# Kernel tuning notes

Measured on AMD Instinct MI355X. Metric: run time of the kernel, lower is better.

Reference implementation:

```python
import jax, jax.numpy as jnp
import numpy as np

# Dimensions (see shape_source): batch, tokens, input dim, attention feature dim, output dim
B, T, D_IN, D_ATTN, D_OUT = 8, 2048, 512, 8, 512
# Weight scale keeps Q,K entries ~N(0, 0.5^2) so scores**power stays finite in fp32
W_SCALE = 0.5 / np.sqrt(D_IN)


def setup_inputs() -> dict:
    key = jax.random.key(0)
    k1, k2, k3, k4 = jax.random.split(key, 4)
    Input = jax.random.normal(k1, (B, T, D_IN), dtype=jnp.float32)
    W_q = jax.random.normal(k2, (D_IN, D_ATTN), dtype=jnp.float32) * W_SCALE
    W_k = jax.random.normal(k3, (D_IN, D_ATTN), dtype=jnp.float32) * W_SCALE
    W_v = jax.random.normal(k4, (D_IN, D_OUT), dtype=jnp.float32) * W_SCALE
    return {"Input": Input, "W_q": W_q, "W_k": W_k, "W_v": W_v, "power": D_ATTN}


def reference(Input, W_q, W_k, W_v, power):
    # QKV projections (torch.mm applied per token)
    Q = jnp.einsum('btd,df->btf', Input, W_q)   # [B,T,D_ATTN]
    K = jnp.einsum('btd,df->btf', Input, W_k)   # [B,T,D_ATTN]
    V = jnp.einsum('btd,do->bto', Input, W_v)   # [B,T,D_OUT]
    # Non-standard score transform: elementwise power by Attention.Feature.Num
    scores = jnp.einsum('btf,bsf->bts', Q, K) ** power  # [B,T,T]
    A = jax.nn.softmax(scores, axis=2)
    # Weighted sum of values
    return jnp.einsum('bts,bso->bto', A, V)  # [B,T,D_OUT]
```

## Files before the change

### kernel.cpp

```cpp
#include <hip/hip_runtime.h>
#include <hip/hip_bf16.h>
#include <stdint.h>


typedef float f32x4_t __attribute__((ext_vector_type(4)));
typedef short s16x8_t __attribute__((ext_vector_type(8)));
typedef unsigned int u32;

static __device__ __forceinline__ unsigned short f2bf(float x){
  union { float f; u32 u; } v; v.f = x;
  return (unsigned short)((v.u + 0x7FFFu + ((v.u >> 16) & 1u)) >> 16);
}

static __device__ __forceinline__ u32 pk2bf(float a, float b){
  __hip_bfloat162 h = __float22bfloat162_rn(float2{a, b});
  union { __hip_bfloat162 h2; u32 u; } c; c.h2 = h;
  return c.u;
}

static __device__ __forceinline__ void gload16(const void* g, void* l){
  __builtin_amdgcn_global_load_lds((const __attribute__((address_space(1))) u32*)g,
                                   (__attribute__((address_space(3))) u32*)l, 16, 0, 0);
}

static __device__ __forceinline__ float rfl(float x){
  return __uint_as_float(__builtin_amdgcn_readfirstlane(__float_as_uint(x)));
}

static __device__ __forceinline__ float dot8(const float* q, const float4& a, const float4& b){
  float s = q[0] * a.x;
  s = fmaf(q[1], a.y, s); s = fmaf(q[2], a.z, s); s = fmaf(q[3], a.w, s);
  s = fmaf(q[4], b.x, s); s = fmaf(q[5], b.y, s); s = fmaf(q[6], b.z, s);
  s = fmaf(q[7], b.w, s);
  return s;
}

__global__ __launch_bounds__(256) void k_wvT(const float* __restrict__ Wv,
                                             unsigned short* __restrict__ WvT){
  __shared__ __align__(16) float tile[64][68];
  const int t = threadIdx.x;
  const int dbase = (blockIdx.x >> 3) * 64;
  const int cbase = (blockIdx.x & 7) * 64;
  {
    const int dl = t >> 2, cq = (t & 3) * 16;
    const float* src = Wv + (size_t)(dbase + dl) * 512 + cbase + cq;
#pragma unroll
    for (int i = 0; i < 16; i += 4){
      float4 v = *(const float4*)(src + i);
      tile[dl][cq + i + 0] = v.x; tile[dl][cq + i + 1] = v.y;
      tile[dl][cq + i + 2] = v.z; tile[dl][cq + i + 3] = v.w;
    }
  }
  __syncthreads();
  const int cl = t >> 2, dq = (t & 3) * 16;
  __align__(16) unsigned short o[16];
#pragma unroll
  for (int i = 0; i < 16; ++i) o[i] = f2bf(tile[dq + i][cl]);
  unsigned short* dst = WvT + (size_t)(cbase + cl) * 512 + dbase + dq;
  *(uint4*)dst = *(const uint4*)o;
  *(uint4*)(dst + 8) = *(const uint4*)(o + 8);
}

__global__ __launch_bounds__(256) void k_fused(const float* __restrict__ In,
                                               const float* __restrict__ Wq,
                                               const float* __restrict__ Wk,
                                               const unsigned short* __restrict__ WvT,
                                               float* __restrict__ Qo,
                                               float* __restrict__ Kt,
                                               unsigned short* __restrict__ Vg){
  __shared__ __align__(16) char smem[65536];
  const int t = threadIdx.x;
  if (blockIdx.x < 1024){
    float* wt = (float*)smem;
    float* inT = (float*)(smem + 32768);
    const float* Inb = In + (size_t)blockIdx.x * 16 * 512;
#pragma unroll
    for (int i = 0; i < 8; ++i)
      gload16(Inb + (i * 256 + t) * 4, (char*)inT + (i * 256 + t) * 16);
#pragma unroll
    for (int i = 0; i < 16; i += 4){
      float4 vq = *(const float4*)(Wq + t * 16 + i);
      float4 vk = *(const float4*)(Wk + t * 16 + i);
      const float* pq = &vq.x;
      const float* pk = &vk.x;
#pragma unroll
      for (int j = 0; j < 4; ++j){
        int flat = t * 16 + i + j;
        int d = flat >> 3, f = flat & 7;
        wt[f * 512 + ((((d >> 2) ^ f) << 2) | (d & 3))] = pq[j];
        int fk = f + 8;
        wt[fk * 512 + ((((d >> 2) ^ (fk & 7)) << 2) | (d & 3))] = pk[j];
      }
    }
    __syncthreads();
    const int tokl = t >> 4;
    const int f = t & 15;
    const float* inrow = inT + tokl * 512;
    const float* wrow = &wt[f * 512];
    const int swz = f & 7;
    double acc = 0.0;
    for (int cb = 0; cb < 128; cb += 8){
      float part = 0.f;
#pragma unroll
      for (int c = cb; c < cb + 8; ++c){
        float4 x = *(const float4*)(inrow + c * 4);
        float4 ww = *(const float4*)(wrow + ((c ^ swz) << 2));
        part = fmaf(x.x, ww.x, part); part = fmaf(x.y, ww.y, part);
        part = fmaf(x.z, ww.z, part); part = fmaf(x.w, ww.w, part);
      }
      acc += (double)part;
    }
    float r = (float)acc;
    const int tok = (int)blockIdx.x * 16 + tokl;
    if (f < 8) Qo[(size_t)tok * 8 + f] = r;
    else {
      const int bq = tok >> 11, kk = tok & 2047;
      const int key = kk & 127, d = f - 8;
      Kt[(size_t)bq * 16384 + (size_t)(kk >> 7) * 1024
         + ((key & 1) * 2 + (d >> 2)) * 256 + (key >> 1) * 4 + (d & 3)] = r;
    }
    return;
  }
  char* Ab = smem;
  char* Bb = smem + 16384;
  char* Img = smem + 32768;
  const int vb = (int)blockIdx.x - 1024;
  const int w = t >> 6, lane = t & 63;
  const int mt = vb >> 2, nt = vb & 3;
  const int wm = w >> 1, wn = w & 1;
  const int asub = lane & 3;
  int arow[2], acr[2];
#pragma unroll
  for (int i = 0; i < 2; ++i){
    arow[i] = (w * 2 + i) * 16 + (lane >> 2);
    acr[i]  = asub ^ ((arow[i] >> 1) & 3);
  }
  f32x4_t acc[4][4];
#pragma unroll
  for (int m = 0; m < 4; ++m)
#pragma unroll
    for (int n = 0; n < 4; ++n)
      acc[m][n] = (f32x4_t){0.f, 0.f, 0.f, 0.f};

  auto stageB = [&](int kk, int sel){
#pragma unroll
    for (int i = 0; i < 2; ++i){
      int id = w * 2 + i;
      const unsigned short* gb = WvT + (size_t)(nt * 128 + arow[i]) * 512 + kk * 32 + acr[i] * 8;
      gload16(gb, Bb + sel * 8192 + id * 1024);
    }
  };
  auto loadA = [&](int kk, float4* x, float4* y){
#pragma unroll
    for (int i = 0; i < 2; ++i){
      const float* ga = In + (size_t)(mt * 128 + arow[i]) * 512 + kk * 32 + acr[i] * 8;
      x[i] = *(const float4*)ga;
      y[i] = *(const float4*)(ga + 4);
    }
  };
  auto writeA = [&](const float4* x, const float4* y, int sel){
#pragma unroll
    for (int i = 0; i < 2; ++i){
      __align__(16) unsigned short pk[8] = {
        f2bf(x[i].x), f2bf(x[i].y), f2bf(x[i].z), f2bf(x[i].w),
        f2bf(y[i].x), f2bf(y[i].y), f2bf(y[i].z), f2bf(y[i].w)};
      *(uint4*)(Ab + sel * 8192 + arow[i] * 64 + asub * 16) = *(const uint4*)pk;
    }
  };
  {
    float4 x[2], y[2];
    loadA(0, x, y);
    stageB(0, 0);
    writeA(x, y, 0);
    __syncthreads();
  }
  for (int kk = 0; kk < 16; ++kk){
    const int cur = kk & 1;
    float4 x[2], y[2];
    if (kk < 15){
      loadA(kk + 1, x, y);
      stageB(kk + 1, cur ^ 1);
    }
    s16x8_t a[4], bf[4];
#pragma unroll
    for (int m = 0; m < 4; ++m){
      int row = wm * 64 + m * 16 + (lane & 15);
      int chn = (lane >> 4) ^ ((row >> 1) & 3);
      a[m] = *(const s16x8_t*)(Ab + cur * 8192 + row * 64 + chn * 16);
    }
#pragma unroll
    for (int n = 0; n < 4; ++n){
      int col = wn * 64 + n * 16 + (lane & 15);
      int chn = (lane >> 4) ^ ((col >> 1) & 3);
      bf[n] = *(const s16x8_t*)(Bb + cur * 8192 + col * 64 + chn * 16);
    }
#pragma unroll
    for (int m = 0; m < 4; ++m)
#pragma unroll
      for (int n = 0; n < 4; ++n)
        acc[m][n] = __builtin_amdgcn_mfma_f32_16x16x32_bf16(a[m], bf[n], acc[m][n], 0, 0, 0);
    if (kk < 15) writeA(x, y, cur ^ 1);
    __syncthreads();
  }
#pragma unroll
  for (int m = 0; m < 4; ++m){
    const int ks2 = (wm * 2 + (m >> 1)) & 3;
    const int hi  = (m * 2 + ((lane >> 4) >> 1)) & 3;
    const int lo0 = ((lane >> 4) & 1) * 4;
#pragma unroll
    for (int n = 0; n < 4; ++n){
      const int g_loc = wn * 2 + (n >> 1);
      const int n2 = n & 1;
      const int cl = lane & 15;
      __align__(8) unsigned short pk2[4];
#pragma unroll
      for (int j = 0; j < 4; ++j) pk2[j] = f2bf(acc[m][n][j]);
      int boff = g_loc * 8192 + n2 * 4096 + ks2 * 1024 + hi * 256 + cl * 16 + lo0 * 2;
      *(uint2*)(Img + boff) = *(const uint2*)pk2;
    }
  }
  __syncthreads();
  const int bq = mt >> 4;
  const int kt = mt & 15;
#pragma unroll
  for (int i = 0; i < 8; ++i){
    int G = i * 256 + t;
    unsigned short* dst = Vg + (size_t)bq * 1048576 + (size_t)kt * 65536
                        + nt * 16384 + G * 8;
    *(uint4*)dst = *(const uint4*)(Img + G * 16);
  }
}

__global__ __launch_bounds__(1024) void k_attn(const float* __restrict__ Qg,
                                               const float* __restrict__ Kt,
                                               const unsigned short* __restrict__ Vg,
                                               float* __restrict__ Out){
  __shared__ __align__(16) char smem[102656];
  const int t = threadIdx.x;
  const int g = t >> 6, lane = t & 63;
  const int b = blockIdx.x & 7;
  const int qt = blockIdx.x >> 3;
  const int qbase = qt * 64;

  float q4[4][8];
#pragma unroll
  for (int rr = 0; rr < 4; ++rr){
    const float* Qp = Qg + (size_t)(b * 2048 + qbase + g * 4 + rr) * 8;
    float4 a = *(const float4*)Qp;
    float4 c = *(const float4*)(Qp + 4);
    q4[rr][0] = rfl(a.x); q4[rr][1] = rfl(a.y); q4[rr][2] = rfl(a.z); q4[rr][3] = rfl(a.w);
    q4[rr][4] = rfl(c.x); q4[rr][5] = rfl(c.y); q4[rr][6] = rfl(c.z); q4[rr][7] = rfl(c.w);
  }
  const float* Kp = Kt + (size_t)b * 16384;
  const unsigned short* Vb = Vg + (size_t)b * 1048576;
  char* Klds = smem;
  char* Pb = smem + 65536;
  float* fin = (float*)(smem + 102400);

#pragma unroll
  for (int i = 0; i < 4; ++i)
    gload16(Kp + (size_t)(i * 1024 + t) * 4, Klds + (i * 1024 + t) * 16);
  __syncthreads();

  float mx0 = 0.f, mx1 = 0.f, mx2 = 0.f, mx3 = 0.f;
  {
    const float* kbase = (const float*)Klds + lane * 4;
#pragma unroll 2
    for (int tt = 0; tt < 16; ++tt){
      const float* kb = kbase + tt * 1024;
      float4 r0 = *(const float4*)(kb);
      float4 r1 = *(const float4*)(kb + 256);
      float4 r2 = *(const float4*)(kb + 512);
      float4 r3 = *(const float4*)(kb + 768);
      {
        float s0 = dot8(q4[0], r0, r1), s1 = dot8(q4[0], r2, r3);
        mx0 = fmaxf(mx0, fmaxf(s0 * s0, s1 * s1));
      }
      {
        float s0 = dot8(q4[1], r0, r1), s1 = dot8(q4[1], r2, r3);
        mx1 = fmaxf(mx1, fmaxf(s0 * s0, s1 * s1));
      }
      {
        float s0 = dot8(q4[2], r0, r1), s1 = dot8(q4[2], r2, r3);
        mx2 = fmaxf(mx2, fmaxf(s0 * s0, s1 * s1));
      }
      {
        float s0 = dot8(q4[3], r0, r1), s1 = dot8(q4[3], r2, r3);
        mx3 = fmaxf(mx3, fmaxf(s0 * s0, s1 * s1));
      }
    }
  }
#pragma unroll
  for (int sh = 1; sh < 64; sh <<= 1){
    mx0 = fmaxf(mx0, __shfl_xor(mx0, sh));
    mx1 = fmaxf(mx1, __shfl_xor(mx1, sh));
    mx2 = fmaxf(mx2, __shfl_xor(mx2, sh));
    mx3 = fmaxf(mx3, __shfl_xor(mx3, sh));
  }
  const float LOG2E = 1.44269504f;
  float nme2_0, nme2_1, nme2_2, nme2_3;
  { float s4 = mx0 * mx0; nme2_0 = rfl(-(s4 * s4) * LOG2E); }
  { float s4 = mx1 * mx1; nme2_1 = rfl(-(s4 * s4) * LOG2E); }
  { float s4 = mx2 * mx2; nme2_2 = rfl(-(s4 * s4) * LOG2E); }
  { float s4 = mx3 * mx3; nme2_3 = rfl(-(s4 * s4) * LOG2E); }
  float lp0 = 0.f, lp1 = 0.f, lp2 = 0.f, lp3 = 0.f;

  f32x4_t acc[4][2];
#pragma unroll
  for (int mm = 0; mm < 4; ++mm)
#pragma unroll
    for (int n = 0; n < 2; ++n)
      acc[mm][n] = (f32x4_t){0.f, 0.f, 0.f, 0.f};

  auto scoreRow = [&](int rr, float nme2r, float& lpr,
                      const float4& r0, const float4& r1,
                      const float4& r2, const float4& r3, int sel){
    float s0 = dot8(q4[rr], r0, r1), s1 = dot8(q4[rr], r2, r3);
    float p0, p1;
    { float a2 = s0 * s0; float a4 = a2 * a2; p0 = a4 * a4; }
    { float a2 = s1 * s1; float a4 = a2 * a2; p1 = a4 * a4; }
    float e0 = __builtin_amdgcn_exp2f(fmaf(p0, LOG2E, nme2r));
    float e1 = __builtin_amdgcn_exp2f(fmaf(p1, LOG2E, nme2r));
    lpr += e0 + e1;
    const int row = g * 4 + rr;
    *(u32*)(Pb + sel * 16384 + row * 256
            + ((((lane >> 2) ^ (row & 15))) << 4) + (lane & 3) * 4) = pk2bf(e0, e1);
  };

  {
    const float* kb = (const float*)Klds + lane * 4;
    float4 r0 = *(const float4*)(kb);
    float4 r1 = *(const float4*)(kb + 256);
    float4 r2 = *(const float4*)(kb + 512);
    float4 r3 = *(const float4*)(kb + 768);
    scoreRow(0, nme2_0, lp0, r0, r1, r2, r3, 0);
    scoreRow(1, nme2_1, lp1, r0, r1, r2, r3, 0);
    scoreRow(2, nme2_2, lp2, r0, r1, r2, r3, 0);
    scoreRow(3, nme2_3, lp3, r0, r1, r2, r3, 0);
  }
  __syncthreads();

  for (int tt = 0; tt < 16; ++tt){
    const int sel = tt & 1;
    s16x8_t vf[2][4];
    {
      const unsigned short* vb = Vb + (size_t)tt * 65536 + g * 4096 + lane * 8;
#pragma unroll
      for (int n = 0; n < 2; ++n)
#pragma unroll
        for (int ks = 0; ks < 4; ++ks)
          vf[n][ks] = *(const s16x8_t*)(vb + n * 2048 + ks * 512);
    }
    const bool more = (tt + 1 < 16);
    float4 r0, r1, r2, r3;
    if (more){
      const float* kb = (const float*)Klds + ((tt + 1) & 15) * 1024 + lane * 4;
      r0 = *(const float4*)(kb);
      r1 = *(const float4*)(kb + 256);
      r2 = *(const float4*)(kb + 512);
      r3 = *(const float4*)(kb + 768);
    }
#pragma unroll
    for (int ks = 0; ks < 4; ++ks){
      if (more){
        if (ks == 0) scoreRow(0, nme2_0, lp0, r0, r1, r2, r3, sel ^ 1);
        if (ks == 1) scoreRow(1, nme2_1, lp1, r0, r1, r2, r3, sel ^ 1);
        if (ks == 2) scoreRow(2, nme2_2, lp2, r0, r1, r2, r3, sel ^ 1);
        if (ks == 3) scoreRow(3, nme2_3, lp3, r0, r1, r2, r3, sel ^ 1);
      }
      s16x8_t a[4];
#pragma unroll
      for (int mm = 0; mm < 4; ++mm){
        int r = mm * 16 + (lane & 15);
        int slot = (ks * 4 + (lane >> 4)) ^ (r & 15);
        a[mm] = *(const s16x8_t*)(Pb + sel * 16384 + r * 256 + (slot << 4));
      }
      __builtin_amdgcn_s_setprio(1);
#pragma unroll
      for (int mm = 0; mm < 4; ++mm)
#pragma unroll
        for (int n = 0; n < 2; ++n)
          acc[mm][n] = __builtin_amdgcn_mfma_f32_16x16x32_bf16(a[mm], vf[n][ks], acc[mm][n], 0, 0, 0);
      __builtin_amdgcn_s_setprio(0);
    }
    __syncthreads();
  }

#pragma unroll
  for (int sh = 1; sh < 64; sh <<= 1){
    lp0 += __shfl_xor(lp0, sh);
    lp1 += __shfl_xor(lp1, sh);
    lp2 += __shfl_xor(lp2, sh);
    lp3 += __shfl_xor(lp3, sh);
  }
  if (lane == 0){
    fin[g * 4 + 0] = 1.f / lp0;
    fin[g * 4 + 1] = 1.f / lp1;
    fin[g * 4 + 2] = 1.f / lp2;
    fin[g * 4 + 3] = 1.f / lp3;
  }
  __syncthreads();

  float* img = (float*)smem;
#pragma unroll
  for (int mm = 0; mm < 4; ++mm){
    float linv[4];
#pragma unroll
    for (int j = 0; j < 4; ++j)
      linv[j] = fin[mm * 16 + ((lane >> 4) << 2) + j];
#pragma unroll
    for (int n = 0; n < 2; ++n){
      int colL = g * 32 + n * 16 + (lane & 15);
#pragma unroll
      for (int j = 0; j < 4; ++j){
        int r16 = ((lane >> 4) << 2) + j;
        img[r16 * 520 + colL] = acc[mm][n][j] * linv[j];
      }
    }
    __syncthreads();
#pragma unroll
    for (int i = 0; i < 2; ++i){
      int f4 = i * 1024 + t;
      int r16 = f4 >> 7, c4 = f4 & 127;
      float4 v = *(const float4*)(img + r16 * 520 + c4 * 4);
      *(float4*)(Out + (size_t)(b * 2048 + qbase + mm * 16 + r16) * 512 + c4 * 4) = v;
    }
    __syncthreads();
  }
}

extern "C" void kernel_launch(void* const* d_in, const int* in_sizes, int n_in,
                              void* d_out, int out_size, void* d_ws, size_t ws_size,
                              hipStream_t stream){
  const float* In = (const float*)d_in[0];
  const float* Wq = (const float*)d_in[1];
  const float* Wk = (const float*)d_in[2];
  const float* Wv = (const float*)d_in[3];
  char* ws = (char*)d_ws;
  unsigned short* WvT = (unsigned short*)(ws);
  float* Q            = (float*)(ws + 524288);
  float* Kt           = (float*)(ws + 1048576);
  unsigned short* Vg  = (unsigned short*)(ws + 1572864);
  float* Out = (float*)d_out;

  hipLaunchKernelGGL(k_wvT,   dim3(64),   dim3(256),  0, stream, Wv, WvT);
  hipLaunchKernelGGL(k_fused, dim3(1536), dim3(256),  0, stream, In, Wq, Wk, WvT, Q, Kt, Vg);
  hipLaunchKernelGGL(k_attn,  dim3(256),  dim3(1024), 0, stream, Q, Kt, Vg, Out);
}
```

Baseline: 97.77 us.

## Replace two-pass max prepass with online softmax rescaling in attention kernel

Removes the separate pass over all keys that computed each row's maximum score. Instead it keeps a running maximum per row, updated with a wave shuffle reduction in every tile. Each tile's correction factor is written to shared memory so the MFMA accumulators can be rescaled before the next tile's accumulation. This trades the prepass's full-length dot products for per-tile shuffles, extra exp2 calls and accumulator multiplies, and it also shrinks shared memory slightly.

```diff
diff --git a/kernel.cpp b/kernel.cpp
--- a/kernel.cpp
+++ b/kernel.cpp
@@ -235,7 +235,7 @@
                                                const float* __restrict__ Kt,
                                                const unsigned short* __restrict__ Vg,
                                                float* __restrict__ Out){
-  __shared__ __align__(16) char smem[102656];
+  __shared__ __align__(16) char smem[99072];
   const int t = threadIdx.x;
   const int g = t >> 6, lane = t & 63;
   const int b = blockIdx.x & 7;
@@ -255,54 +255,16 @@
   const unsigned short* Vb = Vg + (size_t)b * 1048576;
   char* Klds = smem;
   char* Pb = smem + 65536;
-  float* fin = (float*)(smem + 102400);
+  float* facLds = (float*)(smem + 98304);
+  float* fin = (float*)(smem + 98816);
 
 #pragma unroll
   for (int i = 0; i < 4; ++i)
     gload16(Kp + (size_t)(i * 1024 + t) * 4, Klds + (i * 1024 + t) * 16);
   __syncthreads();
 
-  float mx0 = 0.f, mx1 = 0.f, mx2 = 0.f, mx3 = 0.f;
-  {
-    const float* kbase = (const float*)Klds + lane * 4;
-#pragma unroll 2
-    for (int tt = 0; tt < 16; ++tt){
-      const float* kb = kbase + tt * 1024;
-      float4 r0 = *(const float4*)(kb);
-      float4 r1 = *(const float4*)(kb + 256);
-      float4 r2 = *(const float4*)(kb + 512);
-      float4 r3 = *(const float4*)(kb + 768);
-      {
-        float s0 = dot8(q4[0], r0, r1), s1 = dot8(q4[0], r2, r3);
-        mx0 = fmaxf(mx0, fmaxf(s0 * s0, s1 * s1));
-      }
-      {
-        float s0 = dot8(q4[1], r0, r1), s1 = dot8(q4[1], r2, r3);
-        mx1 = fmaxf(mx1, fmaxf(s0 * s0, s1 * s1));
-      }
-      {
-        float s0 = dot8(q4[2], r0, r1), s1 = dot8(q4[2], r2, r3);
-        mx2 = fmaxf(mx2, fmaxf(s0 * s0, s1 * s1));
-      }
-      {
-        float s0 = dot8(q4[3], r0, r1), s1 = dot8(q4[3], r2, r3);
-        mx3 = fmaxf(mx3, fmaxf(s0 * s0, s1 * s1));
-      }
-    }
-  }
-#pragma unroll
-  for (int sh = 1; sh < 64; sh <<= 1){
-    mx0 = fmaxf(mx0, __shfl_xor(mx0, sh));
-    mx1 = fmaxf(mx1, __shfl_xor(mx1, sh));
-    mx2 = fmaxf(mx2, __shfl_xor(mx2, sh));
-    mx3 = fmaxf(mx3, __shfl_xor(mx3, sh));
-  }
   const float LOG2E = 1.44269504f;
-  float nme2_0, nme2_1, nme2_2, nme2_3;
-  { float s4 = mx0 * mx0; nme2_0 = rfl(-(s4 * s4) * LOG2E); }
-  { float s4 = mx1 * mx1; nme2_1 = rfl(-(s4 * s4) * LOG2E); }
-  { float s4 = mx2 * mx2; nme2_2 = rfl(-(s4 * s4) * LOG2E); }
-  { float s4 = mx3 * mx3; nme2_3 = rfl(-(s4 * s4) * LOG2E); }
+  float m0 = 0.f, m1 = 0.f, m2 = 0.f, m3 = 0.f;
   float lp0 = 0.f, lp1 = 0.f, lp2 = 0.f, lp3 = 0.f;
 
   f32x4_t acc[4][2];
@@ -312,17 +274,25 @@
     for (int n = 0; n < 2; ++n)
       acc[mm][n] = (f32x4_t){0.f, 0.f, 0.f, 0.f};
 
-  auto scoreRow = [&](int rr, float nme2r, float& lpr,
+  auto scoreRow = [&](int rr, float& m_rr, float& lpr,
                       const float4& r0, const float4& r1,
                       const float4& r2, const float4& r3, int sel){
     float s0 = dot8(q4[rr], r0, r1), s1 = dot8(q4[rr], r2, r3);
     float p0, p1;
     { float a2 = s0 * s0; float a4 = a2 * a2; p0 = a4 * a4; }
     { float a2 = s1 * s1; float a4 = a2 * a2; p1 = a4 * a4; }
-    float e0 = __builtin_amdgcn_exp2f(fmaf(p0, LOG2E, nme2r));
-    float e1 = __builtin_amdgcn_exp2f(fmaf(p1, LOG2E, nme2r));
-    lpr += e0 + e1;
+    float pm = fmaxf(p0, p1);
+#pragma unroll
+    for (int sh = 1; sh < 64; sh <<= 1) pm = fmaxf(pm, __shfl_xor(pm, sh));
+    float newm = rfl(fmaxf(m_rr, pm));
+    float f = __builtin_amdgcn_exp2f((m_rr - newm) * LOG2E);
+    m_rr = newm;
+    float nm = newm * LOG2E;
+    float e0 = __builtin_amdgcn_exp2f(fmaf(p0, LOG2E, -nm));
+    float e1 = __builtin_amdgcn_exp2f(fmaf(p1, LOG2E, -nm));
+    lpr = fmaf(lpr, f, e0 + e1);
     const int row = g * 4 + rr;
+    if (lane == 0) facLds[sel * 64 + row] = f;
     *(u32*)(Pb + sel * 16384 + row * 256
             + ((((lane >> 2) ^ (row & 15))) << 4) + (lane & 3) * 4) = pk2bf(e0, e1);
   };
@@ -333,10 +303,10 @@
     float4 r1 = *(const float4*)(kb + 256);
     float4 r2 = *(const float4*)(kb + 512);
     float4 r3 = *(const float4*)(kb + 768);
-    scoreRow(0, nme2_0, lp0, r0, r1, r2, r3, 0);
-    scoreRow(1, nme2_1, lp1, r0, r1, r2, r3, 0);
-    scoreRow(2, nme2_2, lp2, r0, r1, r2, r3, 0);
-    scoreRow(3, nme2_3, lp3, r0, r1, r2, r3, 0);
+    scoreRow(0, m0, lp0, r0, r1, r2, r3, 0);
+    scoreRow(1, m1, lp1, r0, r1, r2, r3, 0);
+    scoreRow(2, m2, lp2, r0, r1, r2, r3, 0);
+    scoreRow(3, m3, lp3, r0, r1, r2, r3, 0);
   }
   __syncthreads();
 
@@ -350,6 +320,17 @@
 #pragma unroll
         for (int ks = 0; ks < 4; ++ks)
           vf[n][ks] = *(const s16x8_t*)(vb + n * 2048 + ks * 512);
+    }
+#pragma unroll
+    for (int mm = 0; mm < 4; ++mm){
+      int r0w = mm * 16 + ((lane >> 4) << 2);
+      float4 fc = *(const float4*)(facLds + sel * 64 + r0w);
+      const float* fp = &fc.x;
+#pragma unroll
+      for (int j = 0; j < 4; ++j)
+#pragma unroll
+        for (int n = 0; n < 2; ++n)
+          acc[mm][n][j] *= fp[j];
     }
     const bool more = (tt + 1 < 16);
     float4 r0, r1, r2, r3;
@@ -363,10 +344,10 @@
 #pragma unroll
     for (int ks = 0; ks < 4; ++ks){
       if (more){
-        if (ks == 0) scoreRow(0, nme2_0, lp0, r0, r1, r2, r3, sel ^ 1);
-        if (ks == 1) scoreRow(1, nme2_1, lp1, r0, r1, r2, r3, sel ^ 1);
-        if (ks == 2) scoreRow(2, nme2_2, lp2, r0, r1, r2, r3, sel ^ 1);
-        if (ks == 3) scoreRow(3, nme2_3, lp3, r0, r1, r2, r3, sel ^ 1);
+        if (ks == 0) scoreRow(0, m0, lp0, r0, r1, r2, r3, sel ^ 1);
+        if (ks == 1) scoreRow(1, m1, lp1, r0, r1, r2, r3, sel ^ 1);
+        if (ks == 2) scoreRow(2, m2, lp2, r0, r1, r2, r3, sel ^ 1);
+        if (ks == 3) scoreRow(3, m3, lp3, r0, r1, r2, r3, sel ^ 1);
       }
       s16x8_t a[4];
 #pragma unroll
```

Measured after the change: 124.3 us. 27.1% more time.
